# Kernel tuning notes

Measured on AMD Instinct MI355X. Metric: run time of the kernel, lower is better.

Reference implementation:

```python
import math
import jax, jax.numpy as jnp
import numpy as np

B, T, D_IN, D_SAE, K = 256, 64, 512, 4096, 32

def _sinusoidal_posemb(T, d):
    pos = jnp.arange(T, dtype=jnp.float32)[:, None]
    div = jnp.exp(jnp.arange(0, d, 2, dtype=jnp.float32) * (-(math.log(10000.0) / d)))
    pe = jnp.zeros((T, d), dtype=jnp.float32)
    pe = pe.at[:, 0::2].set(jnp.sin(pos * div))
    pe = pe.at[:, 1::2].set(jnp.cos(pos * div))
    return pe

def setup_inputs() -> dict:
    key = jax.random.key(0)
    k0, k1, k2 = jax.random.split(key, 3)
    x = jax.random.normal(k0, (B, T, D_IN), dtype=jnp.float32)
    W_enc = jax.random.normal(k1, (D_IN, D_SAE), dtype=jnp.float32) / D_IN ** 0.5
    W_dec = jax.random.normal(k2, (D_SAE, T, D_IN), dtype=jnp.float32) / D_SAE ** 0.5
    b_enc = jnp.zeros((D_SAE,), dtype=jnp.float32)
    b_dec = jnp.zeros((T, D_IN), dtype=jnp.float32)
    return {"x": x, "W_enc": W_enc, "W_dec": W_dec, "b_enc": b_enc, "b_dec": b_dec}

def reference(x, W_enc, W_dec, b_enc, b_dec):
    pe = _sinusoidal_posemb(T, D_IN)              # (T, d_in) buffer
    x_plus = x + pe[None]                         # (B, T, d_in)
    pre = jnp.einsum('btd,ds->bs', x_plus, W_enc) + b_enc  # (B, d_sae)
    v, i = jax.lax.top_k(pre, K)                  # (B, K) each
    rows = jnp.arange(B)[:, None]
    z = jnp.zeros_like(pre).at[rows, i].set(jax.nn.relu(v))  # sparse scatter
    x_hat = jnp.einsum('bs,std->btd', z, W_dec) + b_dec      # (B, T, d_in)
    loss = jnp.mean(jnp.sum((x_hat - x) ** 2, axis=-1))
    return loss, x_hat, z
```

## Files before the change

### kernel.cpp

```cpp
#include <hip/hip_runtime.h>
#include <math.h>

#define NB 256
#define NT 64
#define DIN 512
#define DSAE 4096
#define NK 32

__global__ void k_pesum(float* __restrict__ pesum, float* __restrict__ out) {
    int d = threadIdx.x;
    if (d == 0) out[0] = 0.f;
    int j = d >> 1;
    float freq = expf((float)(2 * j) * (-9.210340371976184f / 512.0f));
    float s = 0.f;
    if (d & 1) {
        for (int t = 0; t < NT; ++t) s += cosf((float)t * freq);
    } else {
        for (int t = 0; t < NT; ++t) s += sinf((float)t * freq);
    }
    pesum[d] = s;
}

__global__ void k_xs(const float* __restrict__ x, const float* __restrict__ pesum,
                     float* __restrict__ xs) {
    int b = blockIdx.x, d = threadIdx.x;
    const float* xp = x + (size_t)b * NT * DIN + d;
    float acc = 0.f;
#pragma unroll 16
    for (int t = 0; t < NT; ++t) acc += xp[(size_t)t * DIN];
    xs[(size_t)b * DIN + d] = acc + pesum[d];
}

__global__ __launch_bounds__(256) void k_pre(const float* __restrict__ xs,
                                             const float* __restrict__ W,
                                             const float* __restrict__ b_enc,
                                             float* __restrict__ pre) {
    __shared__ float xs_t[DIN][8];
    const int tid = threadIdx.x;
    const int s = blockIdx.x * 256 + tid;
    const int b0 = blockIdx.y * 8;
    for (int i = tid; i < 8 * DIN; i += 256) {
        int bb = i >> 9, d = i & 511;
        xs_t[d][bb] = xs[(size_t)(b0 + bb) * DIN + d];
    }
    __syncthreads();
    float a0=0,a1=0,a2=0,a3=0,a4=0,a5=0,a6=0,a7=0;
    float c0=0,c1=0,c2=0,c3=0,c4=0,c5=0,c6=0,c7=0;
    const float* wp = W + s;
#pragma unroll 4
    for (int d = 0; d < DIN; d += 2) {
        float w0 = wp[(size_t)d * DSAE];
        float w1 = wp[(size_t)(d + 1) * DSAE];
        float4 lo0 = *(const float4*)&xs_t[d][0];
        float4 hi0 = *(const float4*)&xs_t[d][4];
        float4 lo1 = *(const float4*)&xs_t[d + 1][0];
        float4 hi1 = *(const float4*)&xs_t[d + 1][4];
        a0 += lo0.x * w0; a1 += lo0.y * w0; a2 += lo0.z * w0; a3 += lo0.w * w0;
        a4 += hi0.x * w0; a5 += hi0.y * w0; a6 += hi0.z * w0; a7 += hi0.w * w0;
        c0 += lo1.x * w1; c1 += lo1.y * w1; c2 += lo1.z * w1; c3 += lo1.w * w1;
        c4 += hi1.x * w1; c5 += hi1.y * w1; c6 += hi1.z * w1; c7 += hi1.w * w1;
    }
    float be = b_enc[s];
    pre[(size_t)(b0 + 0) * DSAE + s] = a0 + c0 + be;
    pre[(size_t)(b0 + 1) * DSAE + s] = a1 + c1 + be;
    pre[(size_t)(b0 + 2) * DSAE + s] = a2 + c2 + be;
    pre[(size_t)(b0 + 3) * DSAE + s] = a3 + c3 + be;
    pre[(size_t)(b0 + 4) * DSAE + s] = a4 + c4 + be;
    pre[(size_t)(b0 + 5) * DSAE + s] = a5 + c5 + be;
    pre[(size_t)(b0 + 6) * DSAE + s] = a6 + c6 + be;
    pre[(size_t)(b0 + 7) * DSAE + s] = a7 + c7 + be;
}

__global__ __launch_bounds__(256) void k_topk(const float* __restrict__ pre,
                                              float* __restrict__ z_out,
                                              int* __restrict__ idx_s,
                                              float* __restrict__ zv_s) {
    int b = blockIdx.x, tid = threadIdx.x;
    float* zr = z_out + (size_t)b * DSAE;
    for (int j = tid; j < DSAE; j += 256) zr[j] = 0.f;
    float v[16];
#pragma unroll
    for (int j = 0; j < 16; ++j) v[j] = pre[(size_t)b * DSAE + tid + j * 256];
    __shared__ float s_val[4];
    __shared__ int s_idx[4];
    __shared__ int s_gi;
    __shared__ int all_i[NK];
    __shared__ float all_v[NK];
    for (int k = 0; k < NK; ++k) {
        float bv = -INFINITY; int bi = 0x7fffffff;
#pragma unroll
        for (int j = 0; j < 16; ++j) {
            int ei = tid + j * 256;
            if (v[j] > bv || (v[j] == bv && ei < bi)) { bv = v[j]; bi = ei; }
        }
#pragma unroll
        for (int off = 32; off >= 1; off >>= 1) {
            float ov = __shfl_down(bv, off);
            int oi = __shfl_down(bi, off);
            if (ov > bv || (ov == bv && oi < bi)) { bv = ov; bi = oi; }
        }
        if ((tid & 63) == 0) { s_val[tid >> 6] = bv; s_idx[tid >> 6] = bi; }
        __syncthreads();
        if (tid == 0) {
            float gv = s_val[0]; int gi = s_idx[0];
            for (int w = 1; w < 4; ++w) {
                if (s_val[w] > gv || (s_val[w] == gv && s_idx[w] < gi)) {
                    gv = s_val[w]; gi = s_idx[w];
                }
            }
            s_gi = gi;
            float r = gv > 0.f ? gv : 0.f;
            all_i[k] = gi;
            all_v[k] = r;
            zr[gi] = r;
        }
        __syncthreads();
        int gi = s_gi;
#pragma unroll
        for (int j = 0; j < 16; ++j)
            if (tid + j * 256 == gi) v[j] = -INFINITY;
    }
    if (tid < NK) {
        int myi = all_i[tid]; float myv = all_v[tid];
        int rank = 0;
#pragma unroll
        for (int j = 0; j < NK; ++j) rank += (all_i[j] < myi) ? 1 : 0;
        idx_s[b * NK + rank] = myi;
        zv_s[b * NK + rank] = myv;
    }
}

__global__ __launch_bounds__(256) void k_dec(const float* __restrict__ x,
                                             const float* __restrict__ Wd,
                                             const float* __restrict__ bd,
                                             const int* __restrict__ idx_s,
                                             const float* __restrict__ zv_s,
                                             float* __restrict__ out) {
    const int b = blockIdx.y, chunk = blockIdx.x, tid = threadIdx.x;
    __shared__ int si[NK];
    __shared__ float sz[NK];
    if (tid < NK) { si[tid] = idx_s[b * NK + tid]; sz[tid] = zv_s[b * NK + tid]; }
    __syncthreads();
    const int f0 = chunk * 1024 + tid;
    const float4* bd4 = (const float4*)bd;
    float4 acc0 = bd4[f0];
    float4 acc1 = bd4[f0 + 256];
    float4 acc2 = bd4[f0 + 512];
    float4 acc3 = bd4[f0 + 768];
    for (int k = 0; k < NK; ++k) {
        const float4* w4 = (const float4*)(Wd + (size_t)si[k] * (NT * DIN));
        float zk = sz[k];
        float4 w0 = w4[f0], w1 = w4[f0 + 256], w2 = w4[f0 + 512], w3 = w4[f0 + 768];
        acc0.x += zk * w0.x; acc0.y += zk * w0.y; acc0.z += zk * w0.z; acc0.w += zk * w0.w;
        acc1.x += zk * w1.x; acc1.y += zk * w1.y; acc1.z += zk * w1.z; acc1.w += zk * w1.w;
        acc2.x += zk * w2.x; acc2.y += zk * w2.y; acc2.z += zk * w2.z; acc2.w += zk * w2.w;
        acc3.x += zk * w3.x; acc3.y += zk * w3.y; acc3.z += zk * w3.z; acc3.w += zk * w3.w;
    }
    const float* xr = x + (size_t)b * (NT * DIN);
    float lsum = 0.f, dx;
    float xv[16];
#pragma unroll
    for (int q = 0; q < 4; ++q) {
        int e = (f0 + q * 256) * 4;
#pragma unroll
        for (int c = 0; c < 4; ++c) xv[q * 4 + c] = __builtin_nontemporal_load(&xr[e + c]);
    }
    dx = acc0.x - xv[0];  lsum += dx * dx;  dx = acc0.y - xv[1];  lsum += dx * dx;
    dx = acc0.z - xv[2];  lsum += dx * dx;  dx = acc0.w - xv[3];  lsum += dx * dx;
    dx = acc1.x - xv[4];  lsum += dx * dx;  dx = acc1.y - xv[5];  lsum += dx * dx;
    dx = acc1.z - xv[6];  lsum += dx * dx;  dx = acc1.w - xv[7];  lsum += dx * dx;
    dx = acc2.x - xv[8];  lsum += dx * dx;  dx = acc2.y - xv[9];  lsum += dx * dx;
    dx = acc2.z - xv[10]; lsum += dx * dx;  dx = acc2.w - xv[11]; lsum += dx * dx;
    dx = acc3.x - xv[12]; lsum += dx * dx;  dx = acc3.y - xv[13]; lsum += dx * dx;
    dx = acc3.z - xv[14]; lsum += dx * dx;  dx = acc3.w - xv[15]; lsum += dx * dx;

    float* xh = out + 1 + (size_t)b * (NT * DIN);
    int e;
    e = f0 * 4;
    __builtin_nontemporal_store(acc0.x, &xh[e]);     __builtin_nontemporal_store(acc0.y, &xh[e+1]);
    __builtin_nontemporal_store(acc0.z, &xh[e+2]);   __builtin_nontemporal_store(acc0.w, &xh[e+3]);
    e = (f0 + 256) * 4;
    __builtin_nontemporal_store(acc1.x, &xh[e]);     __builtin_nontemporal_store(acc1.y, &xh[e+1]);
    __builtin_nontemporal_store(acc1.z, &xh[e+2]);   __builtin_nontemporal_store(acc1.w, &xh[e+3]);
    e = (f0 + 512) * 4;
    __builtin_nontemporal_store(acc2.x, &xh[e]);     __builtin_nontemporal_store(acc2.y, &xh[e+1]);
    __builtin_nontemporal_store(acc2.z, &xh[e+2]);   __builtin_nontemporal_store(acc2.w, &xh[e+3]);
    e = (f0 + 768) * 4;
    __builtin_nontemporal_store(acc3.x, &xh[e]);     __builtin_nontemporal_store(acc3.y, &xh[e+1]);
    __builtin_nontemporal_store(acc3.z, &xh[e+2]);   __builtin_nontemporal_store(acc3.w, &xh[e+3]);

#pragma unroll
    for (int off = 32; off >= 1; off >>= 1) lsum += __shfl_down(lsum, off);
    __shared__ float red[4];
    if ((tid & 63) == 0) red[tid >> 6] = lsum;
    __syncthreads();
    if (tid == 0) {
        float tot = red[0] + red[1] + red[2] + red[3];
        atomicAdd(out, tot * (1.0f / (NB * NT)));
    }
}

extern "C" void kernel_launch(void* const* d_in, const int* in_sizes, int n_in,
                              void* d_out, int out_size, void* d_ws, size_t ws_size,
                              hipStream_t stream) {
    const float* x     = (const float*)d_in[0];
    const float* W_enc = (const float*)d_in[1];
    const float* W_dec = (const float*)d_in[2];
    const float* b_enc = (const float*)d_in[3];
    const float* b_dec = (const float*)d_in[4];
    float* out = (float*)d_out;

    float* ws    = (float*)d_ws;
    float* pesum = ws;
    float* xs    = ws + 512;
    float* pre   = ws + 131584;
    int*   idx_s = (int*)(ws + 1180160);
    float* zv_s  = ws + 1188352;

    float* z_out = out + 1 + (size_t)NB * NT * DIN;

    k_pesum<<<1, 512, 0, stream>>>(pesum, out);
    k_xs<<<NB, 512, 0, stream>>>(x, pesum, xs);
    k_pre<<<dim3(16, 32), 256, 0, stream>>>(xs, W_enc, b_enc, pre);
    k_topk<<<NB, 256, 0, stream>>>(pre, z_out, idx_s, zv_s);
    k_dec<<<dim3(8, NB), 256, 0, stream>>>(x, W_dec, b_dec, idx_s, zv_s, out);
}
```

Before: 159.6 us.

## Fuse posemb into xs, widen encoder batch tile, single-wave hierarchical top-k

```diff
diff --git a/kernel.cpp b/kernel.cpp
--- a/kernel.cpp
+++ b/kernel.cpp
@@ -7,126 +7,131 @@
 #define DSAE 4096
 #define NK 32
 
-__global__ void k_pesum(float* __restrict__ pesum, float* __restrict__ out) {
-    int d = threadIdx.x;
-    if (d == 0) out[0] = 0.f;
+__global__ __launch_bounds__(512) void k_xs(const float* __restrict__ x,
+                                            float* __restrict__ xs,
+                                            float* __restrict__ out) {
+    const int b = blockIdx.x, d = threadIdx.x;
+    if (b == 0 && d == 0) out[0] = 0.f;
     int j = d >> 1;
     float freq = expf((float)(2 * j) * (-9.210340371976184f / 512.0f));
-    float s = 0.f;
+    float pes = 0.f;
     if (d & 1) {
-        for (int t = 0; t < NT; ++t) s += cosf((float)t * freq);
+        for (int t = 0; t < NT; ++t) pes += cosf((float)t * freq);
     } else {
-        for (int t = 0; t < NT; ++t) s += sinf((float)t * freq);
-    }
-    pesum[d] = s;
-}
-
-__global__ void k_xs(const float* __restrict__ x, const float* __restrict__ pesum,
-                     float* __restrict__ xs) {
-    int b = blockIdx.x, d = threadIdx.x;
+        for (int t = 0; t < NT; ++t) pes += sinf((float)t * freq);
+    }
     const float* xp = x + (size_t)b * NT * DIN + d;
     float acc = 0.f;
 #pragma unroll 16
     for (int t = 0; t < NT; ++t) acc += xp[(size_t)t * DIN];
-    xs[(size_t)b * DIN + d] = acc + pesum[d];
+    xs[(size_t)b * DIN + d] = acc + pes;
 }
 
 __global__ __launch_bounds__(256) void k_pre(const float* __restrict__ xs,
                                              const float* __restrict__ W,
                                              const float* __restrict__ b_enc,
                                              float* __restrict__ pre) {
-    __shared__ float xs_t[DIN][8];
+    __shared__ float xs_t[DIN][16];
     const int tid = threadIdx.x;
     const int s = blockIdx.x * 256 + tid;
-    const int b0 = blockIdx.y * 8;
-    for (int i = tid; i < 8 * DIN; i += 256) {
+    const int b0 = blockIdx.y * 16;
+    for (int i = tid; i < 16 * DIN; i += 256) {
         int bb = i >> 9, d = i & 511;
         xs_t[d][bb] = xs[(size_t)(b0 + bb) * DIN + d];
     }
     __syncthreads();
-    float a0=0,a1=0,a2=0,a3=0,a4=0,a5=0,a6=0,a7=0;
-    float c0=0,c1=0,c2=0,c3=0,c4=0,c5=0,c6=0,c7=0;
+    float a[16], c[16];
+#pragma unroll
+    for (int i = 0; i < 16; ++i) { a[i] = 0.f; c[i] = 0.f; }
     const float* wp = W + s;
-#pragma unroll 4
+#pragma unroll 2
     for (int d = 0; d < DIN; d += 2) {
         float w0 = wp[(size_t)d * DSAE];
         float w1 = wp[(size_t)(d + 1) * DSAE];
-        float4 lo0 = *(const float4*)&xs_t[d][0];
-        float4 hi0 = *(const float4*)&xs_t[d][4];
-        float4 lo1 = *(const float4*)&xs_t[d + 1][0];
-        float4 hi1 = *(const float4*)&xs_t[d + 1][4];
-        a0 += lo0.x * w0; a1 += lo0.y * w0; a2 += lo0.z * w0; a3 += lo0.w * w0;
-        a4 += hi0.x * w0; a5 += hi0.y * w0; a6 += hi0.z * w0; a7 += hi0.w * w0;
-        c0 += lo1.x * w1; c1 += lo1.y * w1; c2 += lo1.z * w1; c3 += lo1.w * w1;
-        c4 += hi1.x * w1; c5 += hi1.y * w1; c6 += hi1.z * w1; c7 += hi1.w * w1;
+        const float4* r0 = (const float4*)&xs_t[d][0];
+        const float4* r1 = (const float4*)&xs_t[d + 1][0];
+#pragma unroll
+        for (int q = 0; q < 4; ++q) {
+            float4 u = r0[q];
+            a[q*4+0] += u.x * w0; a[q*4+1] += u.y * w0;
+            a[q*4+2] += u.z * w0; a[q*4+3] += u.w * w0;
+            float4 t2 = r1[q];
+            c[q*4+0] += t2.x * w1; c[q*4+1] += t2.y * w1;
+            c[q*4+2] += t2.z * w1; c[q*4+3] += t2.w * w1;
+        }
     }
     float be = b_enc[s];
-    pre[(size_t)(b0 + 0) * DSAE + s] = a0 + c0 + be;
-    pre[(size_t)(b0 + 1) * DSAE + s] = a1 + c1 + be;
-    pre[(size_t)(b0 + 2) * DSAE + s] = a2 + c2 + be;
-    pre[(size_t)(b0 + 3) * DSAE + s] = a3 + c3 + be;
-    pre[(size_t)(b0 + 4) * DSAE + s] = a4 + c4 + be;
-    pre[(size_t)(b0 + 5) * DSAE + s] = a5 + c5 + be;
-    pre[(size_t)(b0 + 6) * DSAE + s] = a6 + c6 + be;
-    pre[(size_t)(b0 + 7) * DSAE + s] = a7 + c7 + be;
-}
-
-__global__ __launch_bounds__(256) void k_topk(const float* __restrict__ pre,
-                                              float* __restrict__ z_out,
-                                              int* __restrict__ idx_s,
-                                              float* __restrict__ zv_s) {
-    int b = blockIdx.x, tid = threadIdx.x;
+#pragma unroll
+    for (int bb = 0; bb < 16; ++bb)
+        pre[(size_t)(b0 + bb) * DSAE + s] = a[bb] + c[bb] + be;
+}
+
+__global__ __launch_bounds__(64) void k_topk(const float* __restrict__ pre,
+                                             float* __restrict__ z_out,
+                                             int* __restrict__ idx_s,
+                                             float* __restrict__ zv_s) {
+    const int b = blockIdx.x, lane = threadIdx.x;
+    const float* pr = pre + (size_t)b * DSAE;
     float* zr = z_out + (size_t)b * DSAE;
-    for (int j = tid; j < DSAE; j += 256) zr[j] = 0.f;
-    float v[16];
-#pragma unroll
-    for (int j = 0; j < 16; ++j) v[j] = pre[(size_t)b * DSAE + tid + j * 256];
-    __shared__ float s_val[4];
-    __shared__ int s_idx[4];
-    __shared__ int s_gi;
-    __shared__ int all_i[NK];
-    __shared__ float all_v[NK];
+    __shared__ float lv[64 * 65];
+    __shared__ float lgv[64 * 8];
+    __shared__ int   lga[64 * 8];
+    for (int j = lane; j < DSAE; j += 64) zr[j] = 0.f;
+    const int base = lane * 65;
+    float v[64];
+#pragma unroll
+    for (int j = 0; j < 64; ++j) v[j] = pr[j * 64 + lane];
+#pragma unroll
+    for (int j = 0; j < 64; ++j) lv[base + j] = v[j];
+    float lmax = -INFINITY; int larg = 0;
+#pragma unroll
+    for (int g = 0; g < 8; ++g) {
+        float m = v[g * 8]; int a = g * 8;
+#pragma unroll
+        for (int t = 1; t < 8; ++t)
+            if (v[g * 8 + t] > m) { m = v[g * 8 + t]; a = g * 8 + t; }
+        lgv[lane * 8 + g] = m; lga[lane * 8 + g] = a;
+        if (m > lmax) { lmax = m; larg = a; }
+    }
+    __syncthreads();
+    int myi = 0; float myv = 0.f;
     for (int k = 0; k < NK; ++k) {
-        float bv = -INFINITY; int bi = 0x7fffffff;
-#pragma unroll
-        for (int j = 0; j < 16; ++j) {
-            int ei = tid + j * 256;
-            if (v[j] > bv || (v[j] == bv && ei < bi)) { bv = v[j]; bi = ei; }
-        }
+        float bv = lmax; int be = larg * 64 + lane;
 #pragma unroll
         for (int off = 32; off >= 1; off >>= 1) {
             float ov = __shfl_down(bv, off);
-            int oi = __shfl_down(bi, off);
-            if (ov > bv || (ov == bv && oi < bi)) { bv = ov; bi = oi; }
+            int oe = __shfl_down(be, off);
+            if (ov > bv || (ov == bv && oe < be)) { bv = ov; be = oe; }
         }
-        if ((tid & 63) == 0) { s_val[tid >> 6] = bv; s_idx[tid >> 6] = bi; }
-        __syncthreads();
-        if (tid == 0) {
-            float gv = s_val[0]; int gi = s_idx[0];
-            for (int w = 1; w < 4; ++w) {
-                if (s_val[w] > gv || (s_val[w] == gv && s_idx[w] < gi)) {
-                    gv = s_val[w]; gi = s_idx[w];
-                }
+        bv = __shfl(bv, 0); be = __shfl(be, 0);
+        if (lane == k) { myi = be; myv = bv > 0.f ? bv : 0.f; }
+        if (lane == (be & 63)) {
+            int j0 = be >> 6;
+            lv[base + j0] = -INFINITY;
+            int g0 = j0 >> 3;
+            float m = -INFINITY; int a2 = g0 << 3;
+            for (int t = 0; t < 8; ++t) {
+                float x2 = lv[base + (g0 << 3) + t];
+                if (x2 > m) { m = x2; a2 = (g0 << 3) + t; }
             }
-            s_gi = gi;
-            float r = gv > 0.f ? gv : 0.f;
-            all_i[k] = gi;
-            all_v[k] = r;
-            zr[gi] = r;
+            lgv[lane * 8 + g0] = m; lga[lane * 8 + g0] = a2;
+            lmax = -INFINITY; larg = 0;
+            for (int g = 0; g < 8; ++g) {
+                float x2 = lgv[lane * 8 + g];
+                if (x2 > lmax) { lmax = x2; larg = lga[lane * 8 + g]; }
+            }
         }
-        __syncthreads();
-        int gi = s_gi;
-#pragma unroll
-        for (int j = 0; j < 16; ++j)
-            if (tid + j * 256 == gi) v[j] = -INFINITY;
-    }
-    if (tid < NK) {
-        int myi = all_i[tid]; float myv = all_v[tid];
-        int rank = 0;
-#pragma unroll
-        for (int j = 0; j < NK; ++j) rank += (all_i[j] < myi) ? 1 : 0;
+    }
+    int rank = 0;
+#pragma unroll
+    for (int j = 0; j < NK; ++j) {
+        int oi = __shfl(myi, j);
+        if (lane < NK && oi < myi) rank++;
+    }
+    if (lane < NK) {
         idx_s[b * NK + rank] = myi;
         zv_s[b * NK + rank] = myv;
+        zr[myi] = myv;
     }
 }
 
@@ -163,7 +168,7 @@
     for (int q = 0; q < 4; ++q) {
         int e = (f0 + q * 256) * 4;
 #pragma unroll
-        for (int c = 0; c < 4; ++c) xv[q * 4 + c] = __builtin_nontemporal_load(&xr[e + c]);
+        for (int c2 = 0; c2 < 4; ++c2) xv[q * 4 + c2] = __builtin_nontemporal_load(&xr[e + c2]);
     }
     dx = acc0.x - xv[0];  lsum += dx * dx;  dx = acc0.y - xv[1];  lsum += dx * dx;
     dx = acc0.z - xv[2];  lsum += dx * dx;  dx = acc0.w - xv[3];  lsum += dx * dx;
@@ -211,17 +216,15 @@
     float* out = (float*)d_out;
 
     float* ws    = (float*)d_ws;
-    float* pesum = ws;
-    float* xs    = ws + 512;
-    float* pre   = ws + 131584;
-    int*   idx_s = (int*)(ws + 1180160);
-    float* zv_s  = ws + 1188352;
+    float* xs    = ws;
+    float* pre   = ws + 131072;
+    int*   idx_s = (int*)(ws + 1179648);
+    float* zv_s  = ws + 1187840;
 
     float* z_out = out + 1 + (size_t)NB * NT * DIN;
 
-    k_pesum<<<1, 512, 0, stream>>>(pesum, out);
-    k_xs<<<NB, 512, 0, stream>>>(x, pesum, xs);
-    k_pre<<<dim3(16, 32), 256, 0, stream>>>(xs, W_enc, b_enc, pre);
-    k_topk<<<NB, 256, 0, stream>>>(pre, z_out, idx_s, zv_s);
+    k_xs<<<NB, 512, 0, stream>>>(x, xs, out);
+    k_pre<<<dim3(16, 16), 256, 0, stream>>>(xs, W_enc, b_enc, pre);
+    k_topk<<<NB, 64, 0, stream>>>(pre, z_out, idx_s, zv_s);
     k_dec<<<dim3(8, NB), 256, 0, stream>>>(x, W_dec, b_dec, idx_s, zv_s, out);
 }
```

Result: faster. 156.2 us (-2.1%).
